# Optimization experiments

Hardware: AMD Instinct MI355X
Metric: run time of the kernel (lower is better)

## Reference

```python
import jax, jax.numpy as jnp
import numpy as np

B, T, N, E = 4, 30, 2000, 32000
F_IN, F_HID, F_GRU, N_CLS = 8, 64, 128, 2


def setup_inputs() -> dict:
    key = jax.random.key(0)
    ks = jax.random.split(key, 12)
    return {
        "x": jax.random.normal(ks[0], (B, T, N, F_IN), jnp.float32),
        "edge_index": jax.random.randint(ks[1], (B, T, 2, E), 0, N, jnp.int32),
        "W1": jax.random.normal(ks[2], (F_IN, F_HID), jnp.float32) * 0.1,
        "b1": jax.random.normal(ks[3], (F_HID,), jnp.float32) * 0.1,
        "W2": jax.random.normal(ks[4], (F_HID, F_HID), jnp.float32) * 0.1,
        "b2": jax.random.normal(ks[5], (F_HID,), jnp.float32) * 0.1,
        "W_ih": jax.random.normal(ks[6], (3 * F_GRU, F_HID), jnp.float32) * 0.1,
        "W_hh": jax.random.normal(ks[7], (3 * F_GRU, F_GRU), jnp.float32) * 0.1,
        "b_ih": jax.random.normal(ks[8], (3 * F_GRU,), jnp.float32) * 0.1,
        "b_hh": jax.random.normal(ks[9], (3 * F_GRU,), jnp.float32) * 0.1,
        "fc_w": jax.random.normal(ks[10], (N_CLS, F_GRU), jnp.float32) * 0.1,
        "fc_b": jax.random.normal(ks[11], (N_CLS,), jnp.float32) * 0.1,
    }


def _gcn_conv(x, src, dst, W, b):
    # PyG GCNConv (edge_weight=None): add self-loops, sym-normalize, x@W, scatter-add, +bias
    n = x.shape[0]
    loops = jnp.arange(n, dtype=src.dtype)
    s = jnp.concatenate([src, loops])
    d = jnp.concatenate([dst, loops])
    deg = jax.ops.segment_sum(jnp.ones(s.shape[0], x.dtype), d, num_segments=n)
    dis = jnp.where(deg > 0, jax.lax.rsqrt(deg), 0.0)
    norm = dis[s] * dis[d]                      # [E+N]
    h = x @ W                                   # [N, Fout]
    msg = h[s] * norm[:, None]                  # gather + scale
    return jax.ops.segment_sum(msg, d, num_segments=n) + b


def _frame_embed(x, ei, W1, b1, W2, b2):
    # one graph frame -> mean-pooled 64-d embedding
    src, dst = ei[0], ei[1]
    h = jax.nn.relu(_gcn_conv(x, src, dst, W1, b1))
    h = jax.nn.relu(_gcn_conv(h, src, dst, W2, b2))
    return h.mean(axis=0)


def _gru(H, W_ih, W_hh, b_ih, b_hh):
    # H: [T, B, F_HID]; torch GRU gate order: r, z, n
    def step(h, x_t):
        gi = x_t @ W_ih.T + b_ih                # [B, 3H]
        gh = h @ W_hh.T + b_hh
        i_r, i_z, i_n = jnp.split(gi, 3, axis=-1)
        h_r, h_z, h_n = jnp.split(gh, 3, axis=-1)
        r = jax.nn.sigmoid(i_r + h_r)
        z = jax.nn.sigmoid(i_z + h_z)
        n = jnp.tanh(i_n + r * h_n)
        h_new = (1.0 - z) * n + z * h
        return h_new, None
    h0 = jnp.zeros((H.shape[1], F_GRU), H.dtype)
    h_final, _ = jax.lax.scan(step, h0, H)
    return h_final                              # [B, F_GRU]


def reference(x, edge_index, W1, b1, W2, b2, W_ih, W_hh, b_ih, b_hh, fc_w, fc_b):
    G = B * T
    xf = x.reshape(G, N, F_IN)
    eif = edge_index.reshape(G, 2, E)
    emb = jax.vmap(_frame_embed, in_axes=(0, 0, None, None, None, None))(
        xf, eif, W1, b1, W2, b2)                # [G, 64]
    H = emb.reshape(B, T, F_HID).transpose(1, 0, 2)  # [T, B, 64]
    h_final = _gru(H, W_ih, W_hh, b_ih, b_hh)   # [B, 128]
    return h_final @ fc_w.T + fc_b              # [B, 2]
```

## Files before the change

kernel.cpp:

```cpp
#include <hip/hip_runtime.h>
#include <math.h>

#define G    120
#define Nn   2000
#define Ee   32000
#define Tt   30
#define Bb   4
#define Fg   128
#define QCAP 9216
#define TSLOT 48

static __device__ __forceinline__ unsigned short f2bf(float f) {
    unsigned u = __float_as_uint(f);
    u += 0x7fffu + ((u >> 16) & 1u);
    return (unsigned short)(u >> 16);
}

#if defined(__has_builtin)
#if __has_builtin(__builtin_amdgcn_cvt_f32_fp8) && __has_builtin(__builtin_amdgcn_cvt_pk_fp8_f32)
#define HW_FP8 1
#endif
#if __has_builtin(__builtin_amdgcn_cvt_pk_f32_fp8)
#define HW_FP8_PK 1
typedef float floatx2 __attribute__((ext_vector_type(2)));
#endif
#endif

static __device__ __forceinline__ unsigned fp8_enc_sw(float x) {
    unsigned s = (__float_as_uint(x) >> 24) & 0x80u;
    float ax = fminf(fabsf(x), 448.f);
    unsigned em;
    if (ax < 0.015625f) {
        em = (unsigned)__float2int_rn(ax * 512.f);
    } else {
        int e = (int)(__float_as_uint(ax) >> 23) - 127;
        float r = ax * __uint_as_float((unsigned)((130 - e) << 23));
        int q = __float2int_rn(r);
        em = (unsigned)(((e + 7) << 3) + (q - 8));
        em = min(em, 126u);
    }
    return s | em;
}
static __device__ __forceinline__ float fp8_dec_sw(unsigned b) {
    unsigned em = b & 0x7fu;
    float mag;
    if (em < 8u) mag = (float)em * 0.001953125f;
    else mag = __uint_as_float((((em >> 3) + 120u) << 23) | ((em & 7u) << 20));
    return (b & 0x80u) ? -mag : mag;
}
static __device__ __forceinline__ unsigned fp8_pack4(float a, float b, float c, float d) {
#ifdef HW_FP8
    int w = __builtin_amdgcn_cvt_pk_fp8_f32(a, b, 0, false);
    w = __builtin_amdgcn_cvt_pk_fp8_f32(c, d, w, true);
    return (unsigned)w;
#else
    return fp8_enc_sw(a) | (fp8_enc_sw(b) << 8) | (fp8_enc_sw(c) << 16) | (fp8_enc_sw(d) << 24);
#endif
}
static __device__ __forceinline__ void fp8x4_dec(unsigned dw, float* o) {
#ifdef HW_FP8_PK
    floatx2 lo = __builtin_amdgcn_cvt_pk_f32_fp8((int)dw, false);
    floatx2 hi = __builtin_amdgcn_cvt_pk_f32_fp8((int)dw, true);
    o[0] = lo[0]; o[1] = lo[1]; o[2] = hi[0]; o[3] = hi[1];
#else
    o[0] = fp8_dec_sw(dw & 0xffu);
    o[1] = fp8_dec_sw((dw >> 8) & 0xffu);
    o[2] = fp8_dec_sw((dw >> 16) & 0xffu);
    o[3] = fp8_dec_sw((dw >> 24) & 0xffu);
#endif
}

__global__ void __launch_bounds__(1024, 1)
k_deg(const int* __restrict__ ei, float* __restrict__ dis, float* __restrict__ emb) {
    __shared__ int hist[Nn];
    int g = blockIdx.x;
    int tid = threadIdx.x;
    for (int idx = tid; idx < Nn; idx += 1024) hist[idx] = 0;
    if (tid < 64) emb[g * 64 + tid] = 0.f;
    __syncthreads();
    const int* dstp = ei + (size_t)g * 2 * Ee + Ee;
    for (int it = tid; it < Ee / 4; it += 1024) {
        int4 d = reinterpret_cast<const int4*>(dstp)[it];
        atomicAdd(&hist[d.x], 1);
        atomicAdd(&hist[d.y], 1);
        atomicAdd(&hist[d.z], 1);
        atomicAdd(&hist[d.w], 1);
    }
    __syncthreads();
    for (int idx = tid; idx < Nn; idx += 1024)
        dis[(size_t)g * Nn + idx] = rsqrtf((float)hist[idx] + 1.0f);
}

__global__ void __launch_bounds__(1024, 1)
k_build(const int* __restrict__ ei, const float* __restrict__ dis,
        int* __restrict__ startA, int* __restrict__ csr,
        unsigned* __restrict__ ellT, int* __restrict__ cntS,
        int* __restrict__ ordS) {
    __shared__ int   histq[500];
    __shared__ float disl[Nn];
    __shared__ int   ws[512];
    __shared__ int   csr_l[QCAP];
    __shared__ int   cntQ[500];
    __shared__ int   exQ[500];
    __shared__ int   nodeAt[500];
    __shared__ int   dh[64];
    __shared__ int   db[64];
    __shared__ int   ovfS;
    int i = blockIdx.x;
    int xcd = i & 7;
    int j = i >> 3;
    int f15 = j >> 2;
    int q = j & 3;
    int g = xcd * 15 + f15;
    int gq = g * 4 + q;
    int lo = q * 500;
    int tid = threadIdx.x;
    for (int idx = tid; idx < Nn; idx += 1024) disl[idx] = dis[(size_t)g * Nn + idx];
    if (tid < 500) histq[tid] = 0;
    if (tid < 64) dh[tid] = 0;
    if (tid == 0) ovfS = 0;
    __syncthreads();
    const int* srcp = ei + (size_t)g * 2 * Ee;
    const int* dstp = srcp + Ee;
    for (int it = tid; it < Ee / 4; it += 1024) {
        int4 d = reinterpret_cast<const int4*>(dstp)[it];
        if ((unsigned)(d.x - lo) < 500u) atomicAdd(&histq[d.x - lo], 1);
        if ((unsigned)(d.y - lo) < 500u) atomicAdd(&histq[d.y - lo], 1);
        if ((unsigned)(d.z - lo) < 500u) atomicAdd(&histq[d.z - lo], 1);
        if ((unsigned)(d.w - lo) < 500u) atomicAdd(&histq[d.w - lo], 1);
    }
    __syncthreads();
    int cnt = 0;
    if (tid < 512) ws[tid] = (tid < 500) ? histq[tid] : 0;
    if (tid < 500) cnt = histq[tid];
    __syncthreads();
    for (int off = 1; off < 512; off <<= 1) {
        int v = 0;
        if (tid < 512 && tid >= off) v = ws[tid - off];
        __syncthreads();
        if (tid < 512) ws[tid] += v;
        __syncthreads();
    }
    int ex = 0;
    if (tid < 500) ex = ws[tid] - cnt;
    if (tid < 500) {
        histq[tid] = ex;
        cntQ[tid] = cnt;
        exQ[tid] = ex;
        if (cnt > TSLOT - 1) atomicMax(&ovfS, 1);
        atomicAdd(&dh[min(cnt, 63)], 1);
    }
    __syncthreads();
    if (tid == 0) {
        int s = 0;
        for (int b = 0; b < 64; ++b) { db[b] = s; s += dh[b]; }
    }
    __syncthreads();
    if (tid < 64) dh[tid] = db[tid];
    __syncthreads();
    if (tid < 500) {
        int p = atomicAdd(&dh[min(cnt, 63)], 1);
        nodeAt[p] = tid;
    }
    for (int it = tid; it < Ee / 4; it += 1024) {
        int4 d = reinterpret_cast<const int4*>(dstp)[it];
        int4 s = reinterpret_cast<const int4*>(srcp)[it];
        if ((unsigned)(d.x - lo) < 500u) { int p = atomicAdd(&histq[d.x - lo], 1); if (p < QCAP) csr_l[p] = s.x; }
        if ((unsigned)(d.y - lo) < 500u) { int p = atomicAdd(&histq[d.y - lo], 1); if (p < QCAP) csr_l[p] = s.y; }
        if ((unsigned)(d.z - lo) < 500u) { int p = atomicAdd(&histq[d.z - lo], 1); if (p < QCAP) csr_l[p] = s.z; }
        if ((unsigned)(d.w - lo) < 500u) { int p = atomicAdd(&histq[d.w - lo], 1); if (p < QCAP) csr_l[p] = s.w; }
    }
    __syncthreads();
    if (tid < 500) {
        int n_own = lo + tid;
        size_t gn_own = (size_t)g * Nn + n_own;
        startA[gn_own] = gq * QCAP + ex;
        int sl = nodeAt[tid];
        int n2 = lo + sl;
        int cnt2 = cntQ[sl];
        int ex2 = exQ[sl];
        int c = q * 500 + tid;
        size_t gc = (size_t)g * Nn + c;
        cntS[gc] = cnt2;
        ordS[gc] = n2;
        float dn2 = disl[n2];
        unsigned* et = ellT + (size_t)g * TSLOT * Nn + c;
        et[0] = (unsigned)n2 | ((unsigned)f2bf(dn2 * dn2) << 16);
        int m2 = min(cnt2, TSLOT - 1);
        for (int e = 0; e < m2; ++e) {
            int s = csr_l[ex2 + e];
            et[(size_t)(e + 1) * Nn] = (unsigned)s | ((unsigned)f2bf(disl[s] * dn2) << 16);
        }
    }
    __syncthreads();
    if (ovfS) {
        int total = ws[511];
        int* cg = csr + (size_t)gq * QCAP;
        for (int it = tid; it < total; it += 1024) cg[it] = csr_l[it];
    }
}

__global__ void __launch_bounds__(256)
k_fused(const float* __restrict__ x, const unsigned* __restrict__ ellT,
        const int* __restrict__ cntS, const int* __restrict__ ordS,
        const int* __restrict__ startA, const int* __restrict__ csr,
        const float* __restrict__ dis,
        const float* __restrict__ W1, const float* __restrict__ b1,
        const float* __restrict__ W2, unsigned char* __restrict__ t2f) {
    int i = blockIdx.x;
    int xcd = i & 7;
    int j = i >> 3;
    int g = xcd * 15 + (j >> 3);
    int blk = j & 7;
    int p = blk * 256 + threadIdx.x;
    bool valid = (p < Nn);
    size_t gp = (size_t)g * Nn + (valid ? p : 0);
    int n = valid ? ordS[gp] : 0;
    int cnt = valid ? cntS[gp] : 0;
    int myc = valid ? (min(cnt, TSLOT - 1) + 1) : 0;
    float aX[8];
#pragma unroll
    for (int k = 0; k < 8; ++k) aX[k] = 0.f;
    {
        const unsigned* et = ellT + (size_t)g * TSLOT * Nn + (valid ? p : 0);
        const float4* x4 = reinterpret_cast<const float4*>(x + (size_t)g * Nn * 8);
        for (int e0 = 0; e0 < TSLOT; e0 += 8) {
            if (!__any(e0 < myc)) break;
            unsigned ub[8];
#pragma unroll
            for (int k = 0; k < 8; ++k)
                ub[k] = (e0 + k < myc) ? et[(size_t)(e0 + k) * Nn] : 0u;
#pragma unroll
            for (int k = 0; k < 8; ++k) {
                if (e0 + k < myc) {
                    float w = __uint_as_float(ub[k] & 0xffff0000u);
                    int s = ub[k] & 0xffffu;
                    float4 r0 = x4[s * 2], r1 = x4[s * 2 + 1];
                    aX[0] += r0.x * w; aX[1] += r0.y * w; aX[2] += r0.z * w; aX[3] += r0.w * w;
                    aX[4] += r1.x * w; aX[5] += r1.y * w; aX[6] += r1.z * w; aX[7] += r1.w * w;
                }
            }
        }
        if (cnt > TSLOT - 1) {
            size_t gn = (size_t)g * Nn + n;
            float dn = dis[gn];
            int start = startA[gn];
            const float* dsg = dis + (size_t)g * Nn;
            for (int e = TSLOT - 1; e < cnt; ++e) {
                int s = csr[start + e];
                float w = dsg[s] * dn;
                float4 r0 = x4[s * 2], r1 = x4[s * 2 + 1];
                aX[0] += r0.x * w; aX[1] += r0.y * w; aX[2] += r0.z * w; aX[3] += r0.w * w;
                aX[4] += r1.x * w; aX[5] += r1.y * w; aX[6] += r1.z * w; aX[7] += r1.w * w;
            }
        }
    }
    float h1r[64];
    {
        const float4* b14 = reinterpret_cast<const float4*>(b1);
#pragma unroll
        for (int f4 = 0; f4 < 16; ++f4) {
            float4 b = b14[f4];
            h1r[4 * f4 + 0] = b.x; h1r[4 * f4 + 1] = b.y;
            h1r[4 * f4 + 2] = b.z; h1r[4 * f4 + 3] = b.w;
        }
        const float4* W14 = reinterpret_cast<const float4*>(W1);
#pragma unroll
        for (int k = 0; k < 8; ++k) {
            float hk = aX[k];
#pragma unroll
            for (int f4 = 0; f4 < 16; ++f4) {
                float4 w = W14[k * 16 + f4];
                h1r[4 * f4 + 0] += hk * w.x; h1r[4 * f4 + 1] += hk * w.y;
                h1r[4 * f4 + 2] += hk * w.z; h1r[4 * f4 + 3] += hk * w.w;
            }
        }
#pragma unroll
        for (int f = 0; f < 64; ++f) h1r[f] = fmaxf(h1r[f], 0.f);
    }
    uint4 oh[2][2];
    {
        const float4* W24 = reinterpret_cast<const float4*>(W2);
#pragma unroll
        for (int hf = 0; hf < 2; ++hf) {
            float acch[32];
#pragma unroll
            for (int f = 0; f < 32; ++f) acch[f] = 0.f;
#pragma unroll
            for (int k = 0; k < 64; ++k) {
                float hk = h1r[k];
#pragma unroll
                for (int f4 = 0; f4 < 8; ++f4) {
                    float4 w = W24[k * 16 + hf * 8 + f4];
                    acch[4 * f4 + 0] += hk * w.x; acch[4 * f4 + 1] += hk * w.y;
                    acch[4 * f4 + 2] += hk * w.z; acch[4 * f4 + 3] += hk * w.w;
                }
            }
            oh[hf][0].x = fp8_pack4(acch[0],  acch[1],  acch[2],  acch[3]);
            oh[hf][0].y = fp8_pack4(acch[4],  acch[5],  acch[6],  acch[7]);
            oh[hf][0].z = fp8_pack4(acch[8],  acch[9],  acch[10], acch[11]);
            oh[hf][0].w = fp8_pack4(acch[12], acch[13], acch[14], acch[15]);
            oh[hf][1].x = fp8_pack4(acch[16], acch[17], acch[18], acch[19]);
            oh[hf][1].y = fp8_pack4(acch[20], acch[21], acch[22], acch[23]);
            oh[hf][1].z = fp8_pack4(acch[24], acch[25], acch[26], acch[27]);
            oh[hf][1].w = fp8_pack4(acch[28], acch[29], acch[30], acch[31]);
        }
    }
    if (valid) {
        uint4* op = reinterpret_cast<uint4*>(t2f + ((size_t)g * Nn + n) * 64);
        op[0] = oh[0][0]; op[1] = oh[0][1]; op[2] = oh[1][0]; op[3] = oh[1][1];
    }
}

__global__ void __launch_bounds__(1024, 1)
k_aggF(const unsigned char* __restrict__ t2f, const unsigned* __restrict__ ellT,
       const int* __restrict__ cntS, const int* __restrict__ ordS,
       const int* __restrict__ startA, const int* __restrict__ csr,
       const float* __restrict__ dis, const float* __restrict__ bias,
       float* __restrict__ emb) {
    __shared__ uint4 stage[Nn * 5];
    int i = blockIdx.x;
    int xcd = i & 7;
    int j = i >> 3;
    int g = xcd * 15 + (j >> 1);
    int half = j & 1;
    int tid = threadIdx.x;
    int w = tid >> 6, lane = tid & 63;
    {
        const uint4* src = reinterpret_cast<const uint4*>(t2f + (size_t)g * Nn * 64);
        for (int it = tid; it < Nn * 4; it += 1024)
            stage[(it >> 2) * 5 + (it & 3)] = src[it];
    }
    __syncthreads();
#define ROWFMA(dw, base) { float o_[4]; fp8x4_dec(dw, o_); \
    acc[base + 0] += o_[0] * wt; acc[base + 1] += o_[1] * wt; \
    acc[base + 2] += o_[2] * wt; acc[base + 3] += o_[3] * wt; }
#define EDGEFMA(s, wt) { \
    uint4 r0 = stage[(s) * 5], r1 = stage[(s) * 5 + 1]; \
    uint4 r2 = stage[(s) * 5 + 2], r3 = stage[(s) * 5 + 3]; \
    ROWFMA(r0.x, 0)  ROWFMA(r0.y, 4)  ROWFMA(r0.z, 8)  ROWFMA(r0.w, 12) \
    ROWFMA(r1.x, 16) ROWFMA(r1.y, 20) ROWFMA(r1.z, 24) ROWFMA(r1.w, 28) \
    ROWFMA(r2.x, 32) ROWFMA(r2.y, 36) ROWFMA(r2.z, 40) ROWFMA(r2.w, 44) \
    ROWFMA(r3.x, 48) ROWFMA(r3.y, 52) ROWFMA(r3.z, 56) ROWFMA(r3.w, 60) }
    int po = w * 64 + lane;
    int p = half * 1000 + po;
    bool valid = (po < 1000);
    size_t gp = (size_t)g * Nn + (valid ? p : 0);
    int cnt = valid ? cntS[gp] : 0;
    int myc = valid ? (min(cnt, TSLOT - 1) + 1) : 0;
    float acc[64];
#pragma unroll
    for (int k = 0; k < 64; ++k) acc[k] = 0.f;
    const unsigned* et = ellT + (size_t)g * TSLOT * Nn + (valid ? p : 0);
    unsigned u_cur = (0 < myc) ? et[0] : 0u;
    for (int e = 0; e < TSLOT; ++e) {
        if (!__any(e < myc)) break;
        unsigned u_nxt = ((e + 1) < TSLOT && (e + 1) < myc)
                             ? et[(size_t)(e + 1) * Nn] : 0u;
        if (e < myc) {
            float wt = __uint_as_float(u_cur & 0xffff0000u);
            int s = u_cur & 0xffffu;
            EDGEFMA(s, wt)
        }
        u_cur = u_nxt;
    }
    if (cnt > TSLOT - 1) {
        int n = ordS[gp];
        size_t gn = (size_t)g * Nn + n;
        float dn = dis[gn];
        int start = startA[gn];
        const float* dsg = dis + (size_t)g * Nn;
        for (int e = TSLOT - 1; e < cnt; ++e) {
            int s = csr[start + e];
            float wt = dsg[s] * dn;
            EDGEFMA(s, wt)
        }
    }
#undef EDGEFMA
#undef ROWFMA
    float pool = 0.f;
#pragma unroll
    for (int k = 0; k < 64; ++k) {
        float v = valid ? fmaxf(acc[k] + bias[k], 0.f) : 0.f;
        v += __shfl_xor(v, 1);  v += __shfl_xor(v, 2);  v += __shfl_xor(v, 4);
        v += __shfl_xor(v, 8);  v += __shfl_xor(v, 16); v += __shfl_xor(v, 32);
        if (lane == k) pool = v;
    }
    atomicAdd(&emb[g * 64 + lane], pool * (1.0f / Nn));
}

__global__ void __launch_bounds__(768, 1)
k_gru_seq(const float* __restrict__ emb, const float* __restrict__ W_ih,
          const float* __restrict__ b_ih, const float* __restrict__ W_hh,
          const float* __restrict__ b_hh, const float* __restrict__ fc_w,
          const float* __restrict__ fc_b, float* __restrict__ out) {
    __shared__ float h[Fg];
    __shared__ float part[768];
    __shared__ float embs[Tt][64];
    __shared__ float pgi[Tt][768];
    int b = blockIdx.x;
    int tid = threadIdx.x;
    int row = tid >> 1;
    int half = tid & 1;
    float w[64];
    const float* wr = W_hh + (size_t)row * Fg + half * 64;
#pragma unroll
    for (int i = 0; i < 64; ++i) w[i] = wr[i];
    float wih[32];
    const float* wir = W_ih + (size_t)row * 64 + half * 32;
#pragma unroll
    for (int i = 0; i < 32; ++i) wih[i] = wir[i];
    for (int it = tid; it < Tt * 64; it += 768)
        embs[it >> 6][it & 63] = emb[((size_t)b * Tt) * 64 + it];
    if (tid < Fg) h[tid] = 0.f;
    __syncthreads();
    for (int t = 0; t < Tt; ++t) {
        const float* e = &embs[t][half * 32];
        float a0 = 0.f, a1 = 0.f, a2 = 0.f, a3 = 0.f;
#pragma unroll
        for (int i = 0; i < 8; ++i) {
            a0 += wih[4 * i + 0] * e[4 * i + 0];
            a1 += wih[4 * i + 1] * e[4 * i + 1];
            a2 += wih[4 * i + 2] * e[4 * i + 2];
            a3 += wih[4 * i + 3] * e[4 * i + 3];
        }
        pgi[t][tid] = (a0 + a1) + (a2 + a3);
    }
    __syncthreads();
    for (int t = 0; t < Tt; ++t) {
        const float* hh = &h[half * 64];
        float a0 = 0.f, a1 = 0.f, a2 = 0.f, a3 = 0.f;
#pragma unroll
        for (int i = 0; i < 16; ++i) {
            a0 += w[4 * i + 0] * hh[4 * i + 0];
            a1 += w[4 * i + 1] * hh[4 * i + 1];
            a2 += w[4 * i + 2] * hh[4 * i + 2];
            a3 += w[4 * i + 3] * hh[4 * i + 3];
        }
        part[tid] = (a0 + a1) + (a2 + a3);
        __syncthreads();
        if (tid < Fg) {
            int j = tid;
            float hr = b_hh[j]       + part[2 * j]           + part[2 * j + 1];
            float hz = b_hh[128 + j] + part[2 * (128 + j)]   + part[2 * (128 + j) + 1];
            float hn = b_hh[256 + j] + part[2 * (256 + j)]   + part[2 * (256 + j) + 1];
            float gr = b_ih[j]       + pgi[t][2 * j]         + pgi[t][2 * j + 1];
            float gz = b_ih[128 + j] + pgi[t][2 * (128 + j)] + pgi[t][2 * (128 + j) + 1];
            float gn = b_ih[256 + j] + pgi[t][2 * (256 + j)] + pgi[t][2 * (256 + j) + 1];
            float r  = 1.f / (1.f + expf(-(gr + hr)));
            float z  = 1.f / (1.f + expf(-(gz + hz)));
            float nn = tanhf(gn + r * hn);
            h[j] = (1.f - z) * nn + z * h[j];
        }
        __syncthreads();
    }
    if (tid < 2) {
        float acc = fc_b[tid];
        for (int k = 0; k < Fg; ++k) acc += fc_w[tid * Fg + k] * h[k];
        out[b * 2 + tid] = acc;
    }
}

extern "C" void kernel_launch(void* const* d_in, const int* in_sizes, int n_in,
                              void* d_out, int out_size, void* d_ws, size_t ws_size,
                              hipStream_t stream) {
    const float* x     = (const float*)d_in[0];
    const int*   ei    = (const int*)  d_in[1];
    const float* W1    = (const float*)d_in[2];
    const float* b1    = (const float*)d_in[3];
    const float* W2    = (const float*)d_in[4];
    const float* b2    = (const float*)d_in[5];
    const float* W_ih  = (const float*)d_in[6];
    const float* W_hh  = (const float*)d_in[7];
    const float* b_ih  = (const float*)d_in[8];
    const float* b_hh  = (const float*)d_in[9];
    const float* fc_w  = (const float*)d_in[10];
    const float* fc_b  = (const float*)d_in[11];
    float* out = (float*)d_out;

    char* ws = (char*)d_ws;
    size_t off = 0;
    auto alloc = [&](size_t bytes) -> void* {
        void* p = ws + off;
        off = (off + bytes + 255) & ~(size_t)255;
        return p;
    };
    float*    dis    = (float*)   alloc((size_t)G * Nn * 4);
    int*      startA = (int*)     alloc((size_t)G * Nn * 4);
    int*      cntS   = (int*)     alloc((size_t)G * Nn * 4);
    int*      ordS   = (int*)     alloc((size_t)G * Nn * 4);
    int*      csr    = (int*)     alloc((size_t)G * 4 * QCAP * 4);
    unsigned* ellT   = (unsigned*)alloc((size_t)G * TSLOT * Nn * 4);
    unsigned char* t2f = (unsigned char*)alloc((size_t)G * Nn * 64);
    float*    emb    = (float*)   alloc((size_t)G * 64 * 4);
    (void)ws_size; (void)in_sizes; (void)n_in; (void)out_size;

    hipLaunchKernelGGL(k_deg,     dim3(G), dim3(1024), 0, stream, ei, dis, emb);
    hipLaunchKernelGGL(k_build,   dim3(480), dim3(1024), 0, stream, ei, dis, startA, csr, ellT, cntS, ordS);
    hipLaunchKernelGGL(k_fused,   dim3(960), dim3(256), 0, stream, x, ellT, cntS, ordS, startA, csr, dis, W1, b1, W2, t2f);
    hipLaunchKernelGGL(k_aggF,    dim3(240), dim3(1024), 0, stream, t2f, ellT, cntS, ordS, startA, csr, dis, b2, emb);
    hipLaunchKernelGGL(k_gru_seq, dim3(Bb), dim3(768), 0, stream, emb, W_ih, b_ih, W_hh, b_hh, fc_w, fc_b, out);
}
```

Baseline: 267.4 us.

## Merge degree and CSR build into one per-graph kernel with full-graph LDS

Folds the degree histogram kernel into the CSR/ELL build kernel, so each block handles a whole graph instead of a quarter. Each block now holds all 32000 edges in LDS (about 160KB) and does a 2000-wide scan. This removes one launch, the dis round trip, and the four-fold re-reading of edge lists per graph. In exchange only 120 blocks run instead of 480, which cuts parallelism, and the larger LDS footprint allows one block per CU.

Result: no change. 266.0 us (-0.5%).

```diff
diff --git a/kernel.cpp b/kernel.cpp
--- a/kernel.cpp
+++ b/kernel.cpp
@@ -71,14 +71,27 @@
 }
 
 __global__ void __launch_bounds__(1024, 1)
-k_deg(const int* __restrict__ ei, float* __restrict__ dis, float* __restrict__ emb) {
-    __shared__ int hist[Nn];
+k_build(const int* __restrict__ ei, float* __restrict__ dis,
+        int* __restrict__ startA, int* __restrict__ csr,
+        unsigned* __restrict__ ellT, int* __restrict__ cntS,
+        int* __restrict__ ordS, float* __restrict__ emb) {
+    __shared__ int   csr_l[Ee];
+    __shared__ int   hist[Nn];
+    __shared__ int   cntL[Nn];
+    __shared__ int   nodeAt[Nn];
+    __shared__ float disl[Nn];
+    __shared__ int   dh[64];
+    __shared__ int   db[64];
+    __shared__ int   ovfS;
     int g = blockIdx.x;
     int tid = threadIdx.x;
     for (int idx = tid; idx < Nn; idx += 1024) hist[idx] = 0;
+    if (tid < 64) dh[tid] = 0;
+    if (tid == 0) ovfS = 0;
     if (tid < 64) emb[g * 64 + tid] = 0.f;
     __syncthreads();
-    const int* dstp = ei + (size_t)g * 2 * Ee + Ee;
+    const int* srcp = ei + (size_t)g * 2 * Ee;
+    const int* dstp = srcp + Ee;
     for (int it = tid; it < Ee / 4; it += 1024) {
         int4 d = reinterpret_cast<const int4*>(dstp)[it];
         atomicAdd(&hist[d.x], 1);
@@ -87,70 +100,25 @@
         atomicAdd(&hist[d.w], 1);
     }
     __syncthreads();
-    for (int idx = tid; idx < Nn; idx += 1024)
-        dis[(size_t)g * Nn + idx] = rsqrtf((float)hist[idx] + 1.0f);
-}
-
-__global__ void __launch_bounds__(1024, 1)
-k_build(const int* __restrict__ ei, const float* __restrict__ dis,
-        int* __restrict__ startA, int* __restrict__ csr,
-        unsigned* __restrict__ ellT, int* __restrict__ cntS,
-        int* __restrict__ ordS) {
-    __shared__ int   histq[500];
-    __shared__ float disl[Nn];
-    __shared__ int   ws[512];
-    __shared__ int   csr_l[QCAP];
-    __shared__ int   cntQ[500];
-    __shared__ int   exQ[500];
-    __shared__ int   nodeAt[500];
-    __shared__ int   dh[64];
-    __shared__ int   db[64];
-    __shared__ int   ovfS;
-    int i = blockIdx.x;
-    int xcd = i & 7;
-    int j = i >> 3;
-    int f15 = j >> 2;
-    int q = j & 3;
-    int g = xcd * 15 + f15;
-    int gq = g * 4 + q;
-    int lo = q * 500;
-    int tid = threadIdx.x;
-    for (int idx = tid; idx < Nn; idx += 1024) disl[idx] = dis[(size_t)g * Nn + idx];
-    if (tid < 500) histq[tid] = 0;
-    if (tid < 64) dh[tid] = 0;
-    if (tid == 0) ovfS = 0;
-    __syncthreads();
-    const int* srcp = ei + (size_t)g * 2 * Ee;
-    const int* dstp = srcp + Ee;
-    for (int it = tid; it < Ee / 4; it += 1024) {
-        int4 d = reinterpret_cast<const int4*>(dstp)[it];
-        if ((unsigned)(d.x - lo) < 500u) atomicAdd(&histq[d.x - lo], 1);
-        if ((unsigned)(d.y - lo) < 500u) atomicAdd(&histq[d.y - lo], 1);
-        if ((unsigned)(d.z - lo) < 500u) atomicAdd(&histq[d.z - lo], 1);
-        if ((unsigned)(d.w - lo) < 500u) atomicAdd(&histq[d.w - lo], 1);
-    }
-    __syncthreads();
-    int cnt = 0;
-    if (tid < 512) ws[tid] = (tid < 500) ? histq[tid] : 0;
-    if (tid < 500) cnt = histq[tid];
-    __syncthreads();
-    for (int off = 1; off < 512; off <<= 1) {
-        int v = 0;
-        if (tid < 512 && tid >= off) v = ws[tid - off];
+    for (int idx = tid; idx < Nn; idx += 1024) {
+        int c = hist[idx];
+        cntL[idx] = c;
+        float dv = rsqrtf((float)c + 1.0f);
+        disl[idx] = dv;
+        dis[(size_t)g * Nn + idx] = dv;
+        atomicAdd(&dh[min(c, 63)], 1);
+        if (c > TSLOT - 1) atomicMax(&ovfS, 1);
+    }
+    __syncthreads();
+    for (int off = 1; off < Nn; off <<= 1) {
+        int i1 = tid + 1024;
+        int v0 = (tid >= off) ? hist[tid - off] : 0;
+        int v1 = (i1 < Nn && i1 >= off) ? hist[i1 - off] : 0;
         __syncthreads();
-        if (tid < 512) ws[tid] += v;
+        hist[tid] += v0;
+        if (i1 < Nn) hist[i1] += v1;
         __syncthreads();
     }
-    int ex = 0;
-    if (tid < 500) ex = ws[tid] - cnt;
-    if (tid < 500) {
-        histq[tid] = ex;
-        cntQ[tid] = cnt;
-        exQ[tid] = ex;
-        if (cnt > TSLOT - 1) atomicMax(&ovfS, 1);
-        atomicAdd(&dh[min(cnt, 63)], 1);
-    }
-    __syncthreads();
     if (tid == 0) {
         int s = 0;
         for (int b = 0; b < 64; ++b) { db[b] = s; s += dh[b]; }
@@ -158,31 +126,29 @@
     __syncthreads();
     if (tid < 64) dh[tid] = db[tid];
     __syncthreads();
-    if (tid < 500) {
-        int p = atomicAdd(&dh[min(cnt, 63)], 1);
-        nodeAt[p] = tid;
-    }
+    for (int idx = tid; idx < Nn; idx += 1024) {
+        int p = atomicAdd(&dh[min(cntL[idx], 63)], 1);
+        nodeAt[p] = idx;
+        hist[idx] -= cntL[idx];
+    }
+    __syncthreads();
     for (int it = tid; it < Ee / 4; it += 1024) {
         int4 d = reinterpret_cast<const int4*>(dstp)[it];
         int4 s = reinterpret_cast<const int4*>(srcp)[it];
-        if ((unsigned)(d.x - lo) < 500u) { int p = atomicAdd(&histq[d.x - lo], 1); if (p < QCAP) csr_l[p] = s.x; }
-        if ((unsigned)(d.y - lo) < 500u) { int p = atomicAdd(&histq[d.y - lo], 1); if (p < QCAP) csr_l[p] = s.y; }
-        if ((unsigned)(d.z - lo) < 500u) { int p = atomicAdd(&histq[d.z - lo], 1); if (p < QCAP) csr_l[p] = s.z; }
-        if ((unsigned)(d.w - lo) < 500u) { int p = atomicAdd(&histq[d.w - lo], 1); if (p < QCAP) csr_l[p] = s.w; }
-    }
-    __syncthreads();
-    if (tid < 500) {
-        int n_own = lo + tid;
-        size_t gn_own = (size_t)g * Nn + n_own;
-        startA[gn_own] = gq * QCAP + ex;
-        int sl = nodeAt[tid];
-        int n2 = lo + sl;
-        int cnt2 = cntQ[sl];
-        int ex2 = exQ[sl];
-        int c = q * 500 + tid;
+        csr_l[atomicAdd(&hist[d.x], 1)] = s.x;
+        csr_l[atomicAdd(&hist[d.y], 1)] = s.y;
+        csr_l[atomicAdd(&hist[d.z], 1)] = s.z;
+        csr_l[atomicAdd(&hist[d.w], 1)] = s.w;
+    }
+    __syncthreads();
+    for (int c = tid; c < Nn; c += 1024) {
+        int n2 = nodeAt[c];
+        int cnt2 = cntL[n2];
+        int ex2 = hist[n2] - cnt2;
         size_t gc = (size_t)g * Nn + c;
         cntS[gc] = cnt2;
         ordS[gc] = n2;
+        startA[(size_t)g * Nn + n2] = g * 4 * QCAP + ex2;
         float dn2 = disl[n2];
         unsigned* et = ellT + (size_t)g * TSLOT * Nn + c;
         et[0] = (unsigned)n2 | ((unsigned)f2bf(dn2 * dn2) << 16);
@@ -194,9 +160,8 @@
     }
     __syncthreads();
     if (ovfS) {
-        int total = ws[511];
-        int* cg = csr + (size_t)gq * QCAP;
-        for (int it = tid; it < total; it += 1024) cg[it] = csr_l[it];
+        int* cg = csr + (size_t)g * 4 * QCAP;
+        for (int it = tid; it < Ee; it += 1024) cg[it] = csr_l[it];
     }
 }
 
@@ -495,8 +460,7 @@
     float*    emb    = (float*)   alloc((size_t)G * 64 * 4);
     (void)ws_size; (void)in_sizes; (void)n_in; (void)out_size;
 
-    hipLaunchKernelGGL(k_deg,     dim3(G), dim3(1024), 0, stream, ei, dis, emb);
-    hipLaunchKernelGGL(k_build,   dim3(480), dim3(1024), 0, stream, ei, dis, startA, csr, ellT, cntS, ordS);
+    hipLaunchKernelGGL(k_build,   dim3(G), dim3(1024), 0, stream, ei, dis, startA, csr, ellT, cntS, ordS, emb);
     hipLaunchKernelGGL(k_fused,   dim3(960), dim3(256), 0, stream, x, ellT, cntS, ordS, startA, csr, dis, W1, b1, W2, t2f);
     hipLaunchKernelGGL(k_aggF,    dim3(240), dim3(1024), 0, stream, t2f, ellT, cntS, ordS, startA, csr, dis, b2, emb);
     hipLaunchKernelGGL(k_gru_seq, dim3(Bb), dim3(768), 0, stream, emb, W_ih, b_ih, W_hh, b_hh, fc_w, fc_b, out);
```
